# Performance work log

Hardware: AMD Instinct MI355X
Metric: run time of the kernel (lower is better)

The kernel has to match this reference:

```python
import jax, jax.numpy as jnp
import numpy as np
import math

B = 2        # batch
S = 4095     # input sequence (cls token makes L = 4096)
F_IN = 32    # input feature size
D = 512      # d_model (hidden_size)
H = 8        # n_heads
E = D // H   # head dim = 64
DFF = 2048   # feedforward dim
NL = 2       # encoder layers
FACTOR = 5   # probsparse sampling factor
EPS = 1e-5


def setup_inputs() -> dict:
    key = jax.random.key(0)
    ks = jax.random.split(key, 16)

    def w(k, shape):
        return jax.random.normal(k, shape, dtype=jnp.float32) * 0.02

    inp = {}
    inp['x'] = jax.random.normal(ks[0], (B, S, F_IN), dtype=jnp.float32)
    inp['We'] = w(ks[1], (D, F_IN)); inp['be'] = jnp.zeros((D,), jnp.float32)
    inp['cls'] = jnp.zeros((1, 1, D), jnp.float32)
    inp['Wq'] = w(ks[2], (NL, D, D)); inp['bq'] = jnp.zeros((NL, D), jnp.float32)
    inp['Wk'] = w(ks[3], (NL, D, D)); inp['bk'] = jnp.zeros((NL, D), jnp.float32)
    inp['Wv'] = w(ks[4], (NL, D, D)); inp['bv'] = jnp.zeros((NL, D), jnp.float32)
    inp['Wo'] = w(ks[5], (NL, D, D)); inp['bo'] = jnp.zeros((NL, D), jnp.float32)
    inp['g1'] = jnp.ones((NL, D), jnp.float32); inp['b1'] = jnp.zeros((NL, D), jnp.float32)
    inp['g2'] = jnp.ones((NL, D), jnp.float32); inp['b2'] = jnp.zeros((NL, D), jnp.float32)
    inp['W1'] = w(ks[6], (NL, DFF, D)); inp['bf1'] = jnp.zeros((NL, DFF), jnp.float32)
    inp['W2'] = w(ks[7], (NL, D, DFF)); inp['bf2'] = jnp.zeros((NL, D), jnp.float32)
    inp['Wf'] = w(ks[8], (1, D)); inp['bf'] = jnp.zeros((1,), jnp.float32)
    return inp


def pos_encoding(L):
    # Sinusoidal positional encoding [L, D]
    pos = jnp.arange(L, dtype=jnp.float32)[:, None]
    div = jnp.exp(jnp.arange(0, D, 2, dtype=jnp.float32) * (-math.log(10000.0) / D))
    pe = jnp.zeros((L, D), jnp.float32)
    pe = pe.at[:, 0::2].set(jnp.sin(pos * div))
    pe = pe.at[:, 1::2].set(jnp.cos(pos * div))
    return pe


def layer_norm(x, g, b):
    mu = x.mean(-1, keepdims=True)
    var = ((x - mu) ** 2).mean(-1, keepdims=True)
    return (x - mu) / jnp.sqrt(var + EPS) * g + b


def prob_attention(q, k, v, rng):
    # q, k, v: [B, H, L, E]; mask_flag=False (encoder self-attention)
    b, h, L, e = q.shape
    u = min(FACTOR * int(np.ceil(np.log(L))), L)  # sample_k == n_top here (L_Q == L_K)
    idx = jax.random.randint(rng, (L, u), 0, L)   # random K sampling per query position
    Ks = k[:, :, idx, :]                          # [B,H,L,u,E] gather
    QKs = jnp.einsum('bhle,bhlue->bhlu', q, Ks)   # sampled scores
    M = QKs.max(-1) - QKs.sum(-1) / L             # sparsity measure [B,H,L]
    _, top = jax.lax.top_k(M, u)                  # active query indices [B,H,u]
    Qr = jnp.take_along_axis(q, top[..., None], axis=2)      # [B,H,u,E]
    scores = jnp.einsum('bhue,bhke->bhuk', Qr, k) / math.sqrt(e)
    attn = jax.nn.softmax(scores, axis=-1)
    ctx = jnp.broadcast_to(v.mean(axis=2, keepdims=True), (b, h, L, e))  # initial context = mean(V)
    upd = jnp.einsum('bhuk,bhke->bhue', attn, v)
    bi = jnp.arange(b)[:, None, None]
    hi = jnp.arange(h)[None, :, None]
    ctx = ctx.at[bi, hi, top].set(upd)            # scatter active-query contexts
    return ctx                                    # [B,H,L,E]


def attention_layer(x, Wq_, bq_, Wk_, bk_, Wv_, bv_, Wo_, bo_, rng):
    b, L, _ = x.shape
    q = (x @ Wq_.T + bq_).reshape(b, L, H, E).transpose(0, 2, 1, 3)
    k = (x @ Wk_.T + bk_).reshape(b, L, H, E).transpose(0, 2, 1, 3)
    v = (x @ Wv_.T + bv_).reshape(b, L, H, E).transpose(0, 2, 1, 3)
    ctx = prob_attention(q, k, v, rng)            # [B,H,L,E]
    out = ctx.transpose(0, 2, 1, 3).reshape(b, L, D)
    return out @ Wo_.T + bo_


def reference(x, We, be, cls, Wq, bq, Wk, bk, Wv, bv, Wo, bo, g1, b1, g2, b2, W1, bf1, W2, bf2, Wf, bf):
    h = x @ We.T + be                                            # [B,S,D]
    h = jnp.concatenate([jnp.broadcast_to(cls, (B, 1, D)), h], axis=1)  # prepend cls
    L = h.shape[1]
    h = h + pos_encoding(L)[None]
    for l in range(NL):
        rng = jax.random.fold_in(jax.random.key(42), l)
        a = attention_layer(h, Wq[l], bq[l], Wk[l], bk[l], Wv[l], bv[l], Wo[l], bo[l], rng)
        h = layer_norm(h + a, g1[l], b1[l])
        y = jax.nn.relu(h @ W1[l].T + bf1[l])
        y = y @ W2[l].T + bf2[l]
        h = layer_norm(h + y, g2[l], b2[l])
    return h[:, 0] @ Wf.T + bf  # cls-token prediction head [B,1]
```

## Files before the change

### kernel.cpp

```cpp
#include <hip/hip_runtime.h>
#include <hip/hip_bf16.h>
#include <math.h>
#include <stdint.h>

#define B 2
#define S 4095
#define LSEQ 4096
#define F_IN 32
#define D 512
#define H 8
#define E 64
#define DFF 2048
#define NL 2
#define U 45
#define EPSL 1e-5f
#define LU (LSEQ * U)
#define HALF_LU (LU / 2)
#define NS 32
#define SLICE 128

typedef __attribute__((ext_vector_type(8))) short short8;
typedef __attribute__((ext_vector_type(4))) float f32x4;

#define GLD(gp, lp)                                                            \
    __builtin_amdgcn_global_load_lds(                                          \
        (const __attribute__((address_space(1))) void*)(gp),                   \
        (__attribute__((address_space(3))) void*)(lp), 16, 0, 0)

__device__ __forceinline__ unsigned short bf16_bits(float f) {
    __hip_bfloat16 h = __float2bfloat16(f);
    return *(unsigned short*)&h;
}
__device__ __forceinline__ float bits_to_f32(unsigned short s) {
    union { uint32_t u; float f; } c;
    c.u = ((uint32_t)s) << 16;
    return c.f;
}
__device__ __forceinline__ unsigned long long mkey(float v, int index) {
    uint32_t u = __float_as_uint(v);
    uint32_t mono = (u & 0x80000000u) ? ~u : (u | 0x80000000u);
    return ((unsigned long long)mono << 32) | (uint32_t)(0xFFFFFFFFu - (uint32_t)index);
}

#define TF_BODY(k0, k1, c0, c1, o0, o1)                                        \
    do {                                                                       \
        uint32_t ks2 = (k0) ^ (k1) ^ 0x1BD11BDAu;                              \
        uint32_t x0 = (c0) + (k0), x1 = (c1) + (k1);                           \
        x0 += x1; x1 = ((x1 << 13) | (x1 >> 19)); x1 ^= x0;                    \
        x0 += x1; x1 = ((x1 << 15) | (x1 >> 17)); x1 ^= x0;                    \
        x0 += x1; x1 = ((x1 << 26) | (x1 >> 6));  x1 ^= x0;                    \
        x0 += x1; x1 = ((x1 << 6) | (x1 >> 26));  x1 ^= x0;                    \
        x0 += (k1); x1 += ks2 + 1u;                                            \
        x0 += x1; x1 = ((x1 << 17) | (x1 >> 15)); x1 ^= x0;                    \
        x0 += x1; x1 = ((x1 << 29) | (x1 >> 3));  x1 ^= x0;                    \
        x0 += x1; x1 = ((x1 << 16) | (x1 >> 16)); x1 ^= x0;                    \
        x0 += x1; x1 = ((x1 << 24) | (x1 >> 8));  x1 ^= x0;                    \
        x0 += ks2; x1 += (k0) + 2u;                                            \
        x0 += x1; x1 = ((x1 << 13) | (x1 >> 19)); x1 ^= x0;                    \
        x0 += x1; x1 = ((x1 << 15) | (x1 >> 17)); x1 ^= x0;                    \
        x0 += x1; x1 = ((x1 << 26) | (x1 >> 6));  x1 ^= x0;                    \
        x0 += x1; x1 = ((x1 << 6) | (x1 >> 26));  x1 ^= x0;                    \
        x0 += (k0); x1 += (k1) + 3u;                                           \
        x0 += x1; x1 = ((x1 << 17) | (x1 >> 15)); x1 ^= x0;                    \
        x0 += x1; x1 = ((x1 << 29) | (x1 >> 3));  x1 ^= x0;                    \
        x0 += x1; x1 = ((x1 << 16) | (x1 >> 16)); x1 ^= x0;                    \
        x0 += x1; x1 = ((x1 << 24) | (x1 >> 8));  x1 ^= x0;                    \
        x0 += (k1); x1 += ks2 + 4u;                                            \
        x0 += x1; x1 = ((x1 << 13) | (x1 >> 19)); x1 ^= x0;                    \
        x0 += x1; x1 = ((x1 << 15) | (x1 >> 17)); x1 ^= x0;                    \
        x0 += x1; x1 = ((x1 << 26) | (x1 >> 6));  x1 ^= x0;                    \
        x0 += x1; x1 = ((x1 << 6) | (x1 >> 26));  x1 ^= x0;                    \
        x0 += ks2; x1 += (k0) + 5u;                                            \
        (o0) = x0; (o1) = x1;                                                  \
    } while (0)

__device__ __forceinline__ void threefry_dev(uint32_t k0, uint32_t k1, uint32_t c0,
                                             uint32_t c1, uint32_t& o0, uint32_t& o1) {
    TF_BODY(k0, k1, c0, c1, o0, o1);
}
static void threefry_host(uint32_t k0, uint32_t k1, uint32_t c0, uint32_t c1,
                          uint32_t& o0, uint32_t& o1) {
    TF_BODY(k0, k1, c0, c1, o0, o1);
}

__global__ void prep_embed_kernel(const float* __restrict__ x, const float* __restrict__ We,
                                  __hip_bfloat16* __restrict__ xbf,
                                  __hip_bfloat16* __restrict__ webf) {
    int u = blockIdx.x * blockDim.x + threadIdx.x;
    const int NX = B * LSEQ * F_IN / 4;
    const int NW = D * F_IN / 4;
    if (u < NX) {
        int e0 = u * 4;
        int i = e0 & 31;
        int l = (e0 >> 5) & (LSEQ - 1);
        int b = e0 >> 17;
        union { unsigned short s[4]; uint2 w; } o;
        if (l == 0) {
            o.s[0] = o.s[1] = o.s[2] = o.s[3] = 0;
        } else {
            float4 v = *(const float4*)(x + ((size_t)b * S + (l - 1)) * F_IN + i);
            o.s[0] = bf16_bits(v.x); o.s[1] = bf16_bits(v.y);
            o.s[2] = bf16_bits(v.z); o.s[3] = bf16_bits(v.w);
        }
        ((uint2*)xbf)[u] = o.w;
    } else if (u < NX + NW) {
        int w = u - NX;
        float4 v = ((const float4*)We)[w];
        union { unsigned short s[4]; uint2 w2; } o;
        o.s[0] = bf16_bits(v.x); o.s[1] = bf16_bits(v.y);
        o.s[2] = bf16_bits(v.z); o.s[3] = bf16_bits(v.w);
        ((uint2*)webf)[w] = o.w2;
    }
}

__global__ __launch_bounds__(256) void gemm32(const unsigned short* __restrict__ A,
                                              const unsigned short* __restrict__ W,
                                              const float* __restrict__ bias,
                                              float* __restrict__ Cf,
                                              int M, int N, int K) {
    __shared__ unsigned short lds[2 * 128 * 32];
    unsigned short* As = lds;
    unsigned short* Bs = lds + 128 * 32;
    const int tid = threadIdx.x;
    const int m0 = blockIdx.y * 128, n0 = blockIdx.x * 128;
    const int wave = tid >> 6, lane = tid & 63;
    const int wm = (wave >> 1) * 64, wn = (wave & 1) * 64;
    const int quad = lane >> 4, m15 = lane & 15;
    const int srow = tid >> 2, scol = (tid & 3) * 8;
    f32x4 acc[4][4] = {};
    const unsigned short* Ag0 = A + (size_t)(m0 + srow) * K + scol;
    const unsigned short* Ag1 = A + (size_t)(m0 + srow + 64) * K + scol;
    const unsigned short* Wg0 = W + (size_t)(n0 + srow) * K + scol;
    const unsigned short* Wg1 = W + (size_t)(n0 + srow + 64) * K + scol;
    for (int k0 = 0; k0 < K; k0 += 32) {
        __syncthreads();
        GLD(Ag0 + k0, As + tid * 8);
        GLD(Ag1 + k0, As + 2048 + tid * 8);
        GLD(Wg0 + k0, Bs + tid * 8);
        GLD(Wg1 + k0, Bs + 2048 + tid * 8);
        __syncthreads();
        short8 af[4], bfr[4];
#pragma unroll
        for (int mi = 0; mi < 4; ++mi)
            af[mi] = *(const short8*)(As + (wm + mi * 16 + m15) * 32 + quad * 8);
#pragma unroll
        for (int ni = 0; ni < 4; ++ni)
            bfr[ni] = *(const short8*)(Bs + (wn + ni * 16 + m15) * 32 + quad * 8);
#pragma unroll
        for (int mi = 0; mi < 4; ++mi)
#pragma unroll
            for (int ni = 0; ni < 4; ++ni)
                acc[mi][ni] = __builtin_amdgcn_mfma_f32_16x16x32_bf16(
                    af[mi], bfr[ni], acc[mi][ni], 0, 0, 0);
    }
#pragma unroll
    for (int mi = 0; mi < 4; ++mi) {
        int mg = m0 + wm + mi * 16 + quad * 4;
#pragma unroll
        for (int ni = 0; ni < 4; ++ni) {
            int ng = n0 + wn + ni * 16 + m15;
            float bv = bias[ng];
#pragma unroll
            for (int r = 0; r < 4; ++r)
                Cf[(size_t)(mg + r) * N + ng] = acc[mi][ni][r] + bv;
        }
    }
}

__global__ void posenc_kernel(const float* __restrict__ emb, const float* __restrict__ cls,
                              __hip_bfloat16* __restrict__ hbf) {
    int gid = blockIdx.x * blockDim.x + threadIdx.x;
    if (gid >= B * LSEQ * D) return;
    int d = gid % D;
    int l = (gid / D) % LSEQ;
    float v = (l == 0) ? cls[d] : emb[gid];
    int i = d >> 1;
    float divv = expf((float)(2 * i) * (float)(-9.210340371976184 / 512.0));
    float ang = (float)l * divv;
    v += (d & 1) ? cosf(ang) : sinf(ang);
    hbf[gid] = __float2bfloat16(v);
}

__global__ void cast_weights_kernel(const float* __restrict__ Wq_l,
                                    const float* __restrict__ Wk_l,
                                    const float* __restrict__ Wv_l,
                                    const float* __restrict__ Wo_l,
                                    const float* __restrict__ W1_l,
                                    const float* __restrict__ W2_l,
                                    const float* __restrict__ bq_l,
                                    const float* __restrict__ bk_l,
                                    const float* __restrict__ bv_l,
                                    __hip_bfloat16* __restrict__ wqb,
                                    __hip_bfloat16* __restrict__ wkb,
                                    __hip_bfloat16* __restrict__ wvb,
                                    __hip_bfloat16* __restrict__ wob,
                                    __hip_bfloat16* __restrict__ w1b,
                                    __hip_bfloat16* __restrict__ w2b,
                                    float* __restrict__ qkvbias,
                                    unsigned char* __restrict__ flags) {
    const int SDD = D * D / 4;
    const int SFD = DFF * D / 4;
    const int CAST_N = 4 * SDD + 2 * SFD;
    int u = blockIdx.x * blockDim.x + threadIdx.x;
    if (u >= CAST_N) {
        int j = u - CAST_N;
        if (j < 384) {
            int seg = (j * 4) >> 9;
            int off = (j * 4) & 511;
            const float* src = (seg == 0) ? bq_l : (seg == 1) ? bk_l : bv_l;
            *(float4*)(qkvbias + j * 4) = *(const float4*)(src + off);
        } else if (j < 384 + B * LSEQ / 4) {
            ((int*)flags)[j - 384] = 0;
        }
        return;
    }
    const float* src;
    __hip_bfloat16* dst;
    int off;
    if (u < SDD) { src = Wq_l; dst = wqb; off = u; }
    else if (u < 2 * SDD) { src = Wk_l; dst = wkb; off = u - SDD; }
    else if (u < 3 * SDD) { src = Wv_l; dst = wvb; off = u - 2 * SDD; }
    else if (u < 4 * SDD) { src = Wo_l; dst = wob; off = u - 3 * SDD; }
    else if (u < 4 * SDD + SFD) { src = W1_l; dst = w1b; off = u - 4 * SDD; }
    else { src = W2_l; dst = w2b; off = u - 4 * SDD - SFD; }
    float4 v = ((const float4*)src)[off];
    union { unsigned short s[4]; uint2 w; } o;
    o.s[0] = bf16_bits(v.x); o.s[1] = bf16_bits(v.y);
    o.s[2] = bf16_bits(v.z); o.s[3] = bf16_bits(v.w);
    ((uint2*)dst)[off] = o.w;
}

template <int MODE>
__global__ __launch_bounds__(256) void gemm_pipe(const unsigned short* __restrict__ A,
                                                 const unsigned short* __restrict__ W,
                                                 const float* __restrict__ bias,
                                                 void* __restrict__ C0,
                                                 void* __restrict__ C1,
                                                 void* __restrict__ C2,
                                                 int M, int N, int K, int NBN) {
    __shared__ unsigned short As[2][128 * 32];
    __shared__ unsigned short Bs[2][128 * 32];
    const int tid = threadIdx.x;
    const int NBM = M >> 7;
    const int bid = blockIdx.x;
    const int xcd = bid & 7, local = bid >> 3;
    const int m_t = xcd * (NBM >> 3) + local / NBN;
    const int n_t = local % NBN;
    const int m0 = m_t * 128, n0 = n_t * 128;
    const int wave = tid >> 6, lane = tid & 63;
    const int wm = (wave >> 1) * 64, wn = (wave & 1) * 64;
    const int quad = lane >> 4, m15 = lane & 15;
    const int srow = tid >> 2, scol = (tid & 3) * 8;
    f32x4 acc[4][4] = {};
    const unsigned short* Ag0 = A + (size_t)(m0 + srow) * K + scol;
    const unsigned short* Ag1 = A + (size_t)(m0 + srow + 64) * K + scol;
    const unsigned short* Wg0 = W + (size_t)(n0 + srow) * K + scol;
    const unsigned short* Wg1 = W + (size_t)(n0 + srow + 64) * K + scol;
    GLD(Ag0, As[0] + tid * 8);
    GLD(Ag1, As[0] + 2048 + tid * 8);
    GLD(Wg0, Bs[0] + tid * 8);
    GLD(Wg1, Bs[0] + 2048 + tid * 8);
    int cur = 0;
    for (int k0 = 0; k0 < K; k0 += 32) {
        __syncthreads();
        int kn = k0 + 32;
        if (kn < K) {
            GLD(Ag0 + kn, As[cur ^ 1] + tid * 8);
            GLD(Ag1 + kn, As[cur ^ 1] + 2048 + tid * 8);
            GLD(Wg0 + kn, Bs[cur ^ 1] + tid * 8);
            GLD(Wg1 + kn, Bs[cur ^ 1] + 2048 + tid * 8);
        }
        short8 af[4], bfr[4];
#pragma unroll
        for (int mi = 0; mi < 4; ++mi)
            af[mi] = *(const short8*)(As[cur] + (wm + mi * 16 + m15) * 32 + quad * 8);
#pragma unroll
        for (int ni = 0; ni < 4; ++ni)
            bfr[ni] = *(const short8*)(Bs[cur] + (wn + ni * 16 + m15) * 32 + quad * 8);
#pragma unroll
        for (int mi = 0; mi < 4; ++mi)
#pragma unroll
            for (int ni = 0; ni < 4; ++ni)
                acc[mi][ni] = __builtin_amdgcn_mfma_f32_16x16x32_bf16(
                    af[mi], bfr[ni], acc[mi][ni], 0, 0, 0);
        cur ^= 1;
    }
#pragma unroll
    for (int mi = 0; mi < 4; ++mi) {
        int mg = m0 + wm + mi * 16 + quad * 4;
#pragma unroll
        for (int ni = 0; ni < 4; ++ni) {
            int ng = n0 + wn + ni * 16 + m15;
            float bv = bias[ng];
#pragma unroll
            for (int r = 0; r < 4; ++r) {
                float v = acc[mi][ni][r] + bv;
                if (MODE == 1) {
                    ((__hip_bfloat16*)C0)[(size_t)(mg + r) * N + ng] = __float2bfloat16(v);
                } else if (MODE == 2) {
                    ((__hip_bfloat16*)C0)[(size_t)(mg + r) * N + ng] =
                        __float2bfloat16(fmaxf(v, 0.f));
                } else {
                    int seg = ng >> 9;
                    int col = ng & 511;
                    __hip_bfloat16* dst = (seg == 0) ? (__hip_bfloat16*)C0
                                        : (seg == 1) ? (__hip_bfloat16*)C1
                                                     : (__hip_bfloat16*)C2;
                    dst[(size_t)(mg + r) * D + col] = __float2bfloat16(v);
                }
            }
        }
    }
}

__global__ __launch_bounds__(256) void gemm_w2b(const unsigned short* __restrict__ A,
                                                const unsigned short* __restrict__ W,
                                                const float* __restrict__ bias,
                                                float* __restrict__ C0,
                                                float* __restrict__ C1) {
    const int K = 2048, N = 512, KH = 1024;
    __shared__ unsigned short As[2][128 * 32];
    __shared__ unsigned short Bs[2][128 * 32];
    const int tid = threadIdx.x;
    const int bid = blockIdx.x;
    const int xcd = bid & 7, local = bid >> 3;
    const int m_t = xcd * 8 + (local >> 3);
    const int n_t = (local >> 1) & 3;
    const int ks = local & 1;
    const int m0 = m_t * 128, n0 = n_t * 128, kb = ks * KH;
    const int wave = tid >> 6, lane = tid & 63;
    const int wm = (wave >> 1) * 64, wn = (wave & 1) * 64;
    const int quad = lane >> 4, m15 = lane & 15;
    const int srow = tid >> 2, scol = (tid & 3) * 8;
    f32x4 acc[4][4] = {};
    const unsigned short* Ag0 = A + (size_t)(m0 + srow) * K + kb + scol;
    const unsigned short* Ag1 = A + (size_t)(m0 + srow + 64) * K + kb + scol;
    const unsigned short* Wg0 = W + (size_t)(n0 + srow) * K + kb + scol;
    const unsigned short* Wg1 = W + (size_t)(n0 + srow + 64) * K + kb + scol;
    GLD(Ag0, As[0] + tid * 8);
    GLD(Ag1, As[0] + 2048 + tid * 8);
    GLD(Wg0, Bs[0] + tid * 8);
    GLD(Wg1, Bs[0] + 2048 + tid * 8);
    int cur = 0;
    for (int k0 = 0; k0 < KH; k0 += 32) {
        __syncthreads();
        int kn = k0 + 32;
        if (kn < KH) {
            GLD(Ag0 + kn, As[cur ^ 1] + tid * 8);
            GLD(Ag1 + kn, As[cur ^ 1] + 2048 + tid * 8);
            GLD(Wg0 + kn, Bs[cur ^ 1] + tid * 8);
            GLD(Wg1 + kn, Bs[cur ^ 1] + 2048 + tid * 8);
        }
        short8 af[4], bfr[4];
#pragma unroll
        for (int mi = 0; mi < 4; ++mi)
            af[mi] = *(const short8*)(As[cur] + (wm + mi * 16 + m15) * 32 + quad * 8);
#pragma unroll
        for (int ni = 0; ni < 4; ++ni)
            bfr[ni] = *(const short8*)(Bs[cur] + (wn + ni * 16 + m15) * 32 + quad * 8);
#pragma unroll
        for (int mi = 0; mi < 4; ++mi)
#pragma unroll
            for (int ni = 0; ni < 4; ++ni)
                acc[mi][ni] = __builtin_amdgcn_mfma_f32_16x16x32_bf16(
                    af[mi], bfr[ni], acc[mi][ni], 0, 0, 0);
        cur ^= 1;
    }
    float* Cf = ks ? C1 : C0;
#pragma unroll
    for (int mi = 0; mi < 4; ++mi) {
        int mg = m0 + wm + mi * 16 + quad * 4;
#pragma unroll
        for (int ni = 0; ni < 4; ++ni) {
            int ng = n0 + wn + ni * 16 + m15;
            float bv = ks ? 0.f : bias[ng];
#pragma unroll
            for (int r = 0; r < 4; ++r)
                Cf[(size_t)(mg + r) * N + ng] = acc[mi][ni][r] + bv;
        }
    }
}

__global__ __launch_bounds__(256) void mscore_kernel(const __hip_bfloat16* __restrict__ qbf,
                                                     const __hip_bfloat16* __restrict__ kbf,
                                                     uint32_t k2a, uint32_t k2b,
                                                     float* __restrict__ Mv) {
    __shared__ float Sbuf[U][8];
    __shared__ int sidx[U];
    int bid = blockIdx.x;
    int b = bid & 1;
    int l = bid >> 1;
    int tid = threadIdx.x;
    int wave = tid >> 6, lane = tid & 63;
    if (tid < U) {
        int i = l * U + tid;
        uint32_t c0 = (i < HALF_LU) ? (uint32_t)i : (uint32_t)(i - HALF_LU);
        uint32_t o0, o1;
        threefry_dev(k2a, k2b, c0, c0 + HALF_LU, o0, o1);
        sidx[tid] = (int)(((i < HALF_LU) ? o0 : o1) & 4095u);
    }
    const unsigned short* qr =
        (const unsigned short*)qbf + ((size_t)(b * LSEQ) + l) * D + lane * 8;
    union { uint4 u; unsigned short s[8]; } qv;
    qv.u = *(const uint4*)qr;
    float qa[8];
#pragma unroll
    for (int j = 0; j < 8; ++j) qa[j] = bits_to_f32(qv.s[j]);
    __syncthreads();
    const unsigned short* kbase = (const unsigned short*)(kbf + (size_t)(b * LSEQ) * D);
    for (int t = wave; t < U; t += 4) {
        int kr = sidx[t];
        union { uint4 u; unsigned short s[8]; } kv;
        kv.u = *(const uint4*)(kbase + (size_t)kr * D + lane * 8);
        float p = 0.f;
#pragma unroll
        for (int j = 0; j < 8; ++j) p += qa[j] * bits_to_f32(kv.s[j]);
        p += __shfl_xor(p, 1);
        p += __shfl_xor(p, 2);
        p += __shfl_xor(p, 4);
        if ((lane & 7) == 0) Sbuf[t][lane >> 3] = p;
    }
    __syncthreads();
    if (tid < 8) {
        float mx = -INFINITY, sm = 0.f;
        for (int t = 0; t < U; ++t) {
            float v = Sbuf[t][tid];
            mx = fmaxf(mx, v);
            sm += v;
        }
        Mv[((size_t)b * H + tid) * LSEQ + l] = mx - sm / (float)LSEQ;
    }
}

__global__ __launch_bounds__(256) void topk_chunk_kernel(const float* __restrict__ Mv,
                                                         unsigned long long* __restrict__ cand) {
    __shared__ unsigned long long sk[256];
    int blk = blockIdx.x;
    int chunk = blk & 15, bh = blk >> 4;
    int tid = threadIdx.x;
    int gi = chunk * 256 + tid;
    sk[tid] = mkey(Mv[(size_t)bh * LSEQ + gi], gi);
    __syncthreads();
    for (int k = 2; k <= 256; k <<= 1) {
        for (int j = k >> 1; j > 0; j >>= 1) {
            int ixj = tid ^ j;
            if (ixj > tid) {
                unsigned long long a = sk[tid], b = sk[ixj];
                bool desc = ((tid & k) == 0);
                if (desc ? (a < b) : (a > b)) { sk[tid] = b; sk[ixj] = a; }
            }
            __syncthreads();
        }
    }
    if (tid < U) cand[((size_t)bh * 16 + chunk) * U + tid] = sk[tid];
}

__global__ __launch_bounds__(256) void topkmerge_vmean_kernel(
        const unsigned long long* __restrict__ cand, int* __restrict__ top,
        const __hip_bfloat16* __restrict__ v, float* __restrict__ part) {
    __shared__ unsigned long long sk[1024];
    __shared__ float red[4][64];
    int blk = blockIdx.x;
    int tid = threadIdx.x;
    if (blk < B * H) {
        int bh = blk;
        for (int e = tid; e < 1024; e += 256)
            sk[e] = (e < 16 * U) ? cand[(size_t)bh * 16 * U + e] : 0ull;
        __syncthreads();
        for (int k = 2; k <= 1024; k <<= 1) {
            for (int j = k >> 1; j > 0; j >>= 1) {
                for (int e = tid; e < 1024; e += 256) {
                    int ixj = e ^ j;
                    if (ixj > e) {
                        unsigned long long a = sk[e], b = sk[ixj];
                        bool desc = ((e & k) == 0);
                        if (desc ? (a < b) : (a > b)) { sk[e] = b; sk[ixj] = a; }
                    }
                }
                __syncthreads();
            }
        }
        if (tid < U)
            top[bh * U + tid] = (int)(0xFFFFFFFFu - (uint32_t)(sk[tid] & 0xFFFFFFFFu));
    } else {
        int vb = blk - B * H;
        int seg = vb & 7, hh = (vb >> 3) & 7, b = vb >> 6;
        int e = tid & 63, rg = tid >> 6;
        const __hip_bfloat16* vp =
            v + ((size_t)(b * LSEQ) + seg * 512) * D + hh * 64 + e;
        float acc = 0.f;
        for (int r = rg; r < 512; r += 4) acc += __bfloat162float(vp[(size_t)r * D]);
        red[rg][e] = acc;
        __syncthreads();
        if (tid < 64)
            part[(size_t)vb * 64 + tid] =
                red[0][tid] + red[1][tid] + red[2][tid] + red[3][tid];
    }
}

__global__ __launch_bounds__(256) void zero_wobase_kernel(
        const int* __restrict__ top, float* __restrict__ aout,
        unsigned char* __restrict__ flags, const float* __restrict__ vpart,
        const unsigned short* __restrict__ wob, const float* __restrict__ bo,
        float* __restrict__ base) {
    int bid = blockIdx.x;
    int tid = threadIdx.x;
    if (bid < B * H * U) {
        int t = bid % U;
        int bh = bid / U;
        int b = bh >> 3;
        int r = top[bh * U + t];
        if (tid < 128) {
            float4 z = {0.f, 0.f, 0.f, 0.f};
            ((float4*)(aout + (size_t)(b * LSEQ + r) * D))[tid] = z;
        }
        if (tid == 0) flags[b * LSEQ + r] = 1;
    } else {
        int wb = bid - B * H * U;
        int b = wb >> 7;
        int n = (wb & 127) * 4 + (tid >> 6);
        int lane = tid & 63;
        float vmv[8];
#pragma unroll
        for (int j = 0; j < 8; ++j) {
            int idx = lane * 8 + j;
            int hh = idx >> 6, e = idx & 63;
            float acc = 0.f;
#pragma unroll
            for (int s = 0; s < 8; ++s)
                acc += vpart[((size_t)(b * 8 + hh) * 8 + s) * 64 + e];
            vmv[j] = acc / (float)LSEQ;
        }
        union { uint4 u; unsigned short s[8]; } w;
        w.u = *(const uint4*)(wob + (size_t)n * D + lane * 8);
        float p = vmv[0] * bits_to_f32(w.s[0]) + vmv[1] * bits_to_f32(w.s[1]) +
                  vmv[2] * bits_to_f32(w.s[2]) + vmv[3] * bits_to_f32(w.s[3]) +
                  vmv[4] * bits_to_f32(w.s[4]) + vmv[5] * bits_to_f32(w.s[5]) +
                  vmv[6] * bits_to_f32(w.s[6]) + vmv[7] * bits_to_f32(w.s[7]);
        for (int off = 32; off; off >>= 1) p += __shfl_xor(p, off);
        if (lane == 0) base[(size_t)b * D + n] = p + bo[n];
    }
}

__global__ __launch_bounds__(256) void attnred_corr_kernel(const float* __restrict__ Opart,
                                                           const float* __restrict__ msum,
                                                           const float* __restrict__ vpart,
                                                           const unsigned short* __restrict__ wob,
                                                           const int* __restrict__ top,
                                                           float* __restrict__ aout) {
    __shared__ float dlt[E];
    int bid = blockIdx.x;
    int t = bid % U;
    int bh = bid / U;
    int b = bh >> 3, hh = bh & 7;
    int tid = threadIdx.x;
    if (tid < 64) {
        int lane = tid;
        float m_s = -INFINITY, ss = 0.f;
        if (lane < NS) {
            size_t base = (((size_t)bh * NS + lane) * U + t) * 2;
            m_s = msum[base];
            ss = msum[base + 1];
        }
        float M = m_s;
        for (int off = 32; off; off >>= 1) M = fmaxf(M, __shfl_xor(M, off));
        float e_s = (lane < NS) ? __expf(m_s - M) : 0.f;
        float d = ss * e_s;
        for (int off = 32; off; off >>= 1) d += __shfl_xor(d, off);
        float acc = 0.f;
        for (int s = 0; s < NS; ++s) {
            float w = __shfl(e_s, s);
            acc += w * Opart[(((size_t)bh * NS + s) * U + t) * 64 + lane];
        }
        float vmv = 0.f;
#pragma unroll
        for (int s = 0; s < 8; ++s) vmv += vpart[((size_t)bh * 8 + s) * 64 + lane];
        dlt[lane] = acc / d - vmv / (float)LSEQ;
    }
    __syncthreads();
    int r = top[bh * U + t];
    float* arow = aout + (size_t)(b * LSEQ + r) * D;
    for (int n = tid; n < D; n += 256) {
        const unsigned short* wr = wob + (size_t)n * D + hh * E;
        float acc = 0.f;
#pragma unroll
        for (int k2 = 0; k2 < E; ++k2) acc += dlt[k2] * bits_to_f32(wr[k2]);
        atomicAdd(arow + n, acc);
    }
}

__global__ __launch_bounds__(256) void attn_part(const __hip_bfloat16* __restrict__ qbf,
                                                 const __hip_bfloat16* __restrict__ kbf,
                                                 const __hip_bfloat16* __restrict__ vbf,
                                                 const int* __restrict__ top,
                                                 float* __restrict__ Opart,
                                                 float* __restrict__ msum) {
    __shared__ unsigned short Qs[48 * 72];
    __shared__ unsigned short Ks[SLICE * 72];
    __shared__ unsigned short Vs[SLICE * 68];
    __shared__ unsigned short Ps[48 * 136];
    __shared__ float mred[48][4];
    __shared__ float sred[48][4];
    const int slice = blockIdx.x, hh = blockIdx.y, b = blockIdx.z;
    const int bh = b * H + hh;
    const int tid = threadIdx.x;
    const int s0 = slice * SLICE;
    for (int i = tid; i < 48 * 64; i += 256) {
        int t = i >> 6, e = i & 63;
        unsigned short v = 0;
        if (t < U) {
            int r = top[bh * U + t];
            v = ((const unsigned short*)qbf)[((size_t)(b * LSEQ) + r) * D + hh * E + e];
        }
        Qs[t * 72 + e] = v;
    }
    {
        const uint4* src = (const uint4*)(kbf + ((size_t)(b * LSEQ) + s0) * D + hh * E);
        for (int i = tid; i < SLICE * 8; i += 256) {
            int r = i >> 3, c = i & 7;
            uint4 d = src[(size_t)r * 64 + c];
            *(uint4*)(Ks + r * 72 + c * 8) = d;
        }
    }
    {
        const uint2* src = (const uint2*)(vbf + ((size_t)(b * LSEQ) + s0) * D + hh * E);
        for (int i = tid; i < SLICE * 16; i += 256) {
            int r = i >> 4, c = i & 15;
            uint2 d = src[(size_t)r * 128 + c];
            *(uint2*)(Vs + r * 68 + c * 4) = d;
        }
    }
    __syncthreads();
    const int wave = tid >> 6, lane = tid & 63;
    const int quad = lane >> 4, m15 = lane & 15;
    const int wc = wave * 32;
    f32x4 acc[3][2] = {};
#pragma unroll
    for (int ks = 0; ks < 2; ++ks) {
        short8 af[3], bfr[2];
#pragma unroll
        for (int mt = 0; mt < 3; ++mt)
            af[mt] = *(const short8*)(Qs + (mt * 16 + m15) * 72 + ks * 32 + quad * 8);
#pragma unroll
        for (int nt = 0; nt < 2; ++nt)
            bfr[nt] = *(const short8*)(Ks + (wc + nt * 16 + m15) * 72 + ks * 32 + quad * 8);
#pragma unroll
        for (int mt = 0; mt < 3; ++mt)
#pragma unroll
            for (int nt = 0; nt < 2; ++nt)
                acc[mt][nt] = __builtin_amdgcn_mfma_f32_16x16x32_bf16(
                    af[mt], bfr[nt], acc[mt][nt], 0, 0, 0);
    }
    float sc[3][2][4];
#pragma unroll
    for (int mt = 0; mt < 3; ++mt)
#pragma unroll
        for (int nt = 0; nt < 2; ++nt)
#pragma unroll
            for (int r = 0; r < 4; ++r) sc[mt][nt][r] = acc[mt][nt][r] * 0.125f;
#pragma unroll
    for (int mt = 0; mt < 3; ++mt)
#pragma unroll
        for (int r = 0; r < 4; ++r) {
            float mv = fmaxf(sc[mt][0][r], sc[mt][1][r]);
            mv = fmaxf(mv, __shfl_xor(mv, 1));
            mv = fmaxf(mv, __shfl_xor(mv, 2));
            mv = fmaxf(mv, __shfl_xor(mv, 4));
            mv = fmaxf(mv, __shfl_xor(mv, 8));
            if (m15 == 0) mred[mt * 16 + quad * 4 + r][wave] = mv;
        }
    __syncthreads();
#pragma unroll
    for (int mt = 0; mt < 3; ++mt)
#pragma unroll
        for (int r = 0; r < 4; ++r) {
            int row = mt * 16 + quad * 4 + r;
            float ms = fmaxf(fmaxf(mred[row][0], mred[row][1]),
                             fmaxf(mred[row][2], mred[row][3]));
            float p0 = __expf(sc[mt][0][r] - ms);
            float p1 = __expf(sc[mt][1][r] - ms);
            float sv = p0 + p1;
            sv += __shfl_xor(sv, 1);
            sv += __shfl_xor(sv, 2);
            sv += __shfl_xor(sv, 4);
            sv += __shfl_xor(sv, 8);
            if (m15 == 0) sred[row][wave] = sv;
            Ps[row * 136 + wc + m15] = bf16_bits(p0);
            Ps[row * 136 + wc + 16 + m15] = bf16_bits(p1);
        }
    __syncthreads();
    if (tid < U) {
        float mm = fmaxf(fmaxf(mred[tid][0], mred[tid][1]),
                         fmaxf(mred[tid][2], mred[tid][3]));
        float ss = sred[tid][0] + sred[tid][1] + sred[tid][2] + sred[tid][3];
        size_t base = (((size_t)bh * NS + slice) * U + tid) * 2;
        msum[base] = mm;
        msum[base + 1] = ss;
    }
    f32x4 apv[3] = {};
#pragma unroll
    for (int ks = 0; ks < 4; ++ks) {
        short8 bv;
#pragma unroll
        for (int j = 0; j < 8; ++j)
            bv[j] = (short)Vs[(ks * 32 + quad * 8 + j) * 68 + wave * 16 + m15];
        short8 af2[3];
#pragma unroll
        for (int mt = 0; mt < 3; ++mt)
            af2[mt] = *(const short8*)(Ps + (mt * 16 + m15) * 136 + ks * 32 + quad * 8);
#pragma unroll
        for (int mt = 0; mt < 3; ++mt)
            apv[mt] = __builtin_amdgcn_mfma_f32_16x16x32_bf16(af2[mt], bv, apv[mt], 0, 0, 0);
    }
    size_t obase = ((size_t)bh * NS + slice) * U;
#pragma unroll
    for (int mt = 0; mt < 3; ++mt)
#pragma unroll
        for (int r = 0; r < 4; ++r) {
            int row = mt * 16 + quad * 4 + r;
            if (row < U)
                Opart[(obase + row) * 64 + wave * 16 + m15] = apv[mt][r];
        }
}

__global__ __launch_bounds__(64) void add_ln_base_kernel(__hip_bfloat16* __restrict__ hbf,
                                                         const float* __restrict__ base,
                                                         const float* __restrict__ aout,
                                                         const unsigned char* __restrict__ flags,
                                                         const float* __restrict__ g,
                                                         const float* __restrict__ bb) {
    int row = blockIdx.x;
    int b = row >> 12;
    int lane = threadIdx.x;
    unsigned short* hp = (unsigned short*)hbf + (size_t)row * D;
    const float* bp = base + (size_t)b * D;
    const float* ap = aout + (size_t)row * D;
    bool has = flags[row] != 0;
    float x[8];
    float sum = 0.f;
#pragma unroll
    for (int j = 0; j < 8; ++j) {
        float a = bp[lane + 64 * j];
        if (has) a += ap[lane + 64 * j];
        x[j] = bits_to_f32(hp[lane + 64 * j]) + a;
        sum += x[j];
    }
    for (int off = 32; off; off >>= 1) sum += __shfl_xor(sum, off);
    float mu = sum / (float)D;
    float vs = 0.f;
#pragma unroll
    for (int j = 0; j < 8; ++j) {
        float dd = x[j] - mu;
        vs += dd * dd;
    }
    for (int off = 32; off; off >>= 1) vs += __shfl_xor(vs, off);
    float inv = 1.f / sqrtf(vs / (float)D + EPSL);
#pragma unroll
    for (int j = 0; j < 8; ++j) {
        float o = (x[j] - mu) * inv * g[lane + 64 * j] + bb[lane + 64 * j];
        hp[lane + 64 * j] = bf16_bits(o);
    }
}

__global__ __launch_bounds__(64) void add_ln_kernel(__hip_bfloat16* __restrict__ hbf,
                                                    const float* __restrict__ a,
                                                    const float* __restrict__ a2,
                                                    const float* __restrict__ g,
                                                    const float* __restrict__ bb) {
    int row = blockIdx.x;
    int lane = threadIdx.x;
    unsigned short* hp = (unsigned short*)hbf + (size_t)row * D;
    const float* ap = a + (size_t)row * D;
    const float* ap2 = a2 + (size_t)row * D;
    float x[8];
    float sum = 0.f;
#pragma unroll
    for (int j = 0; j < 8; ++j) {
        x[j] = bits_to_f32(hp[lane + 64 * j]) + ap[lane + 64 * j] + ap2[lane + 64 * j];
        sum += x[j];
    }
    for (int off = 32; off; off >>= 1) sum += __shfl_xor(sum, off);
    float mu = sum / (float)D;
    float vs = 0.f;
#pragma unroll
    for (int j = 0; j < 8; ++j) {
        float dd = x[j] - mu;
        vs += dd * dd;
    }
    for (int off = 32; off; off >>= 1) vs += __shfl_xor(vs, off);
    float inv = 1.f / sqrtf(vs / (float)D + EPSL);
#pragma unroll
    for (int j = 0; j < 8; ++j) {
        float o = (x[j] - mu) * inv * g[lane + 64 * j] + bb[lane + 64 * j];
        hp[lane + 64 * j] = bf16_bits(o);
    }
}

__global__ void final_kernel(const __hip_bfloat16* __restrict__ hbf,
                             const float* __restrict__ Wf,
                             const float* __restrict__ bf, float* __restrict__ out) {
    int b = blockIdx.x;
    int lane = threadIdx.x;
    const unsigned short* hp = (const unsigned short*)hbf + (size_t)b * LSEQ * D;
    float acc = 0.f;
    for (int j = lane; j < D; j += 64) acc += bits_to_f32(hp[j]) * Wf[j];
    for (int off = 32; off; off >>= 1) acc += __shfl_xor(acc, off);
    if (lane == 0) out[b] = acc + bf[0];
}

extern "C" void kernel_launch(void* const* d_in, const int* in_sizes, int n_in,
                              void* d_out, int out_size, void* d_ws, size_t ws_size,
                              hipStream_t stream) {
    (void)in_sizes; (void)n_in; (void)out_size; (void)ws_size;
    const float* x   = (const float*)d_in[0];
    const float* We  = (const float*)d_in[1];
    const float* be  = (const float*)d_in[2];
    const float* cls = (const float*)d_in[3];
    const float* Wq  = (const float*)d_in[4];
    const float* bq  = (const float*)d_in[5];
    const float* Wk  = (const float*)d_in[6];
    const float* bk  = (const float*)d_in[7];
    const float* Wv  = (const float*)d_in[8];
    const float* bv  = (const float*)d_in[9];
    const float* Wo  = (const float*)d_in[10];
    const float* bo  = (const float*)d_in[11];
    const float* g1  = (const float*)d_in[12];
    const float* b1  = (const float*)d_in[13];
    const float* g2  = (const float*)d_in[14];
    const float* b2  = (const float*)d_in[15];
    const float* W1  = (const float*)d_in[16];
    const float* bf1 = (const float*)d_in[17];
    const float* W2  = (const float*)d_in[18];
    const float* bf2 = (const float*)d_in[19];
    const float* Wf  = (const float*)d_in[20];
    const float* bff = (const float*)d_in[21];
    float* out = (float*)d_out;

    float* ws = (float*)d_ws;
    const size_t NT = (size_t)B * LSEQ * D;
    float* aout = ws + NT;
    __hip_bfloat16* kbf    = (__hip_bfloat16*)(ws + NT);
    __hip_bfloat16* q_bf   = (__hip_bfloat16*)(ws + 2 * NT);
    __hip_bfloat16* y1_bf  = (__hip_bfloat16*)(ws + 2 * NT);
    __hip_bfloat16* v_bf   = (__hip_bfloat16*)(ws + 4 * NT);
    __hip_bfloat16* h_bf   = (__hip_bfloat16*)(ws + 5 * NT);
    float* emb  = ws;
    float* tmp  = ws;
    float* Opart = ws + 3 * NT;
    float* msumb = Opart + (size_t)B * H * NS * U * 64;
    float* wpool = ws + 5 * NT + NT / 2;
    __hip_bfloat16* wqb = (__hip_bfloat16*)wpool;
    __hip_bfloat16* wkb = wqb + (size_t)D * D;
    __hip_bfloat16* wvb = wkb + (size_t)D * D;
    __hip_bfloat16* wob = wvb + (size_t)D * D;
    __hip_bfloat16* w1b = wob + (size_t)D * D;
    __hip_bfloat16* w2b = w1b + (size_t)DFF * D;
    float* after_w = wpool + ((size_t)4 * D * D + 2 * (size_t)DFF * D) / 2;
    float* Mbuf = after_w;
    int* top    = (int*)(Mbuf + (size_t)B * H * LSEQ);
    float* vm   = (float*)(top + B * H * U);
    float* vpart  = vm + (size_t)B * H * E;
    float* baseb  = vpart + (size_t)128 * 64;
    __hip_bfloat16* xbf  = (__hip_bfloat16*)(baseb + (size_t)B * D);
    __hip_bfloat16* webf = xbf + (size_t)B * LSEQ * F_IN;
    unsigned long long* cand =
        (unsigned long long*)(((uintptr_t)(webf + (size_t)D * F_IN) + 7) & ~(uintptr_t)7);
    float* qkvbias = (float*)(cand + (size_t)B * H * 16 * U);
    unsigned char* flags = (unsigned char*)(qkvbias + 1536);

    const int ML = B * LSEQ;
    dim3 gD(D / 128, ML / 128);
    const int CAST_N = 4 * (D * D / 4) + 2 * (DFF * D / 4);
    const int CAST_TOT = CAST_N + 384 + B * LSEQ / 4;

    prep_embed_kernel<<<(B * LSEQ * F_IN / 4 + D * F_IN / 4 + 255) / 256, 256, 0, stream>>>(
        x, We, xbf, webf);
    gemm32<<<gD, 256, 0, stream>>>((const unsigned short*)xbf,
                                   (const unsigned short*)webf, be, emb, ML, D, F_IN);
    posenc_kernel<<<(B * LSEQ * D + 255) / 256, 256, 0, stream>>>(emb, cls, h_bf);

    for (int l = 0; l < NL; ++l) {
        uint32_t f0, f1, a0, a1, bb0, bb1;
        threefry_host(0u, 42u, 0u, (uint32_t)l, f0, f1);
        threefry_host(f0, f1, 0u, 2u, a0, a1);
        threefry_host(f0, f1, 1u, 3u, bb0, bb1);
        (void)a0; (void)bb0;

        cast_weights_kernel<<<(CAST_TOT + 255) / 256, 256, 0, stream>>>(
            Wq + (size_t)l * D * D, Wk + (size_t)l * D * D, Wv + (size_t)l * D * D,
            Wo + (size_t)l * D * D, W1 + (size_t)l * DFF * D, W2 + (size_t)l * D * DFF,
            bq + l * D, bk + l * D, bv + l * D,
            wqb, wkb, wvb, wob, w1b, w2b, qkvbias, flags);

        gemm_pipe<3><<<768, 256, 0, stream>>>((const unsigned short*)h_bf,
                                              (const unsigned short*)wqb, qkvbias,
                                              q_bf, kbf, v_bf, ML, 3 * D, D, 12);

        mscore_kernel<<<B * LSEQ, 256, 0, stream>>>(q_bf, kbf, a1, bb1, Mbuf);
        topk_chunk_kernel<<<B * H * 16, 256, 0, stream>>>(Mbuf, cand);
        topkmerge_vmean_kernel<<<B * H + B * H * 8, 256, 0, stream>>>(cand, top, v_bf,
                                                                      vpart);
        attn_part<<<dim3(NS, H, B), 256, 0, stream>>>(q_bf, kbf, v_bf, top, Opart, msumb);
        zero_wobase_kernel<<<B * H * U + B * 128, 256, 0, stream>>>(
            top, aout, flags, vpart, (const unsigned short*)wob, bo + l * D, baseb);
        attnred_corr_kernel<<<B * H * U, 256, 0, stream>>>(Opart, msumb, vpart,
                                                           (const unsigned short*)wob, top,
                                                           aout);
        add_ln_base_kernel<<<ML, 64, 0, stream>>>(h_bf, baseb, aout, flags,
                                                  g1 + l * D, b1 + l * D);

        gemm_pipe<2><<<1024, 256, 0, stream>>>((const unsigned short*)h_bf,
                                               (const unsigned short*)w1b, bf1 + l * DFF,
                                               y1_bf, nullptr, nullptr, ML, DFF, D, 16);
        gemm_w2b<<<512, 256, 0, stream>>>((const unsigned short*)y1_bf,
                                          (const unsigned short*)w2b, bf2 + l * D,
                                          aout, tmp);
        add_ln_kernel<<<ML, 64, 0, stream>>>(h_bf, aout, tmp, g2 + l * D, b2 + l * D);
    }

    final_kernel<<<B, 64, 0, stream>>>(h_bf, Wf, bff, out);
}
```

Baseline: 553.0 us.

## Hoist weight casting for both layers into one launch and batch K-row loads

Weight and bias casting for both layers now runs in a single 2D-grid launch before the layer loop, with per-layer bf16 slices in a larger pool. This removes one kernel launch per layer. The flag zeroing moves into extra blocks of the top-k merge kernel. The mscore kernel issues three sampled-K row loads per iteration before reducing them, to hide memory latency, and the Wo correction loop reads 16-byte vectors instead of scalars. The weight pool grows to hold both layers.

```diff
diff --git a/kernel.cpp b/kernel.cpp
--- a/kernel.cpp
+++ b/kernel.cpp
@@ -181,48 +181,44 @@
     hbf[gid] = __float2bfloat16(v);
 }
 
-__global__ void cast_weights_kernel(const float* __restrict__ Wq_l,
-                                    const float* __restrict__ Wk_l,
-                                    const float* __restrict__ Wv_l,
-                                    const float* __restrict__ Wo_l,
-                                    const float* __restrict__ W1_l,
-                                    const float* __restrict__ W2_l,
-                                    const float* __restrict__ bq_l,
-                                    const float* __restrict__ bk_l,
-                                    const float* __restrict__ bv_l,
-                                    __hip_bfloat16* __restrict__ wqb,
-                                    __hip_bfloat16* __restrict__ wkb,
-                                    __hip_bfloat16* __restrict__ wvb,
-                                    __hip_bfloat16* __restrict__ wob,
-                                    __hip_bfloat16* __restrict__ w1b,
-                                    __hip_bfloat16* __restrict__ w2b,
-                                    float* __restrict__ qkvbias,
-                                    unsigned char* __restrict__ flags) {
+__global__ void cast_weights_kernel(const float* __restrict__ Wq,
+                                    const float* __restrict__ Wk,
+                                    const float* __restrict__ Wv,
+                                    const float* __restrict__ Wo,
+                                    const float* __restrict__ W1,
+                                    const float* __restrict__ W2,
+                                    const float* __restrict__ bq,
+                                    const float* __restrict__ bk,
+                                    const float* __restrict__ bv,
+                                    __hip_bfloat16* __restrict__ wpool,
+                                    float* __restrict__ qkvbias) {
     const int SDD = D * D / 4;
     const int SFD = DFF * D / 4;
     const int CAST_N = 4 * SDD + 2 * SFD;
+    const size_t WPL = (size_t)4 * D * D + 2 * (size_t)DFF * D;
+    int l = blockIdx.y;
     int u = blockIdx.x * blockDim.x + threadIdx.x;
+    __hip_bfloat16* base = wpool + (size_t)l * WPL;
     if (u >= CAST_N) {
         int j = u - CAST_N;
         if (j < 384) {
             int seg = (j * 4) >> 9;
             int off = (j * 4) & 511;
-            const float* src = (seg == 0) ? bq_l : (seg == 1) ? bk_l : bv_l;
-            *(float4*)(qkvbias + j * 4) = *(const float4*)(src + off);
-        } else if (j < 384 + B * LSEQ / 4) {
-            ((int*)flags)[j - 384] = 0;
+            const float* src = (seg == 0) ? bq + l * D
+                             : (seg == 1) ? bk + l * D : bv + l * D;
+            *(float4*)(qkvbias + l * 1536 + j * 4) = *(const float4*)(src + off);
         }
         return;
     }
     const float* src;
     __hip_bfloat16* dst;
     int off;
-    if (u < SDD) { src = Wq_l; dst = wqb; off = u; }
-    else if (u < 2 * SDD) { src = Wk_l; dst = wkb; off = u - SDD; }
-    else if (u < 3 * SDD) { src = Wv_l; dst = wvb; off = u - 2 * SDD; }
-    else if (u < 4 * SDD) { src = Wo_l; dst = wob; off = u - 3 * SDD; }
-    else if (u < 4 * SDD + SFD) { src = W1_l; dst = w1b; off = u - 4 * SDD; }
-    else { src = W2_l; dst = w2b; off = u - 4 * SDD - SFD; }
+    if (u < SDD)            { src = Wq + (size_t)l * D * D;   dst = base;                       off = u; }
+    else if (u < 2 * SDD)   { src = Wk + (size_t)l * D * D;   dst = base + (size_t)D * D;       off = u - SDD; }
+    else if (u < 3 * SDD)   { src = Wv + (size_t)l * D * D;   dst = base + (size_t)2 * D * D;   off = u - 2 * SDD; }
+    else if (u < 4 * SDD)   { src = Wo + (size_t)l * D * D;   dst = base + (size_t)3 * D * D;   off = u - 3 * SDD; }
+    else if (u < 4 * SDD + SFD) { src = W1 + (size_t)l * DFF * D; dst = base + (size_t)4 * D * D; off = u - 4 * SDD; }
+    else { src = W2 + (size_t)l * D * DFF; dst = base + (size_t)4 * D * D + (size_t)DFF * D; off = u - 4 * SDD - SFD; }
     float4 v = ((const float4*)src)[off];
     union { unsigned short s[4]; uint2 w; } o;
     o.s[0] = bf16_bits(v.x); o.s[1] = bf16_bits(v.y);
@@ -408,17 +404,40 @@
     for (int j = 0; j < 8; ++j) qa[j] = bits_to_f32(qv.s[j]);
     __syncthreads();
     const unsigned short* kbase = (const unsigned short*)(kbf + (size_t)(b * LSEQ) * D);
-    for (int t = wave; t < U; t += 4) {
-        int kr = sidx[t];
-        union { uint4 u; unsigned short s[8]; } kv;
-        kv.u = *(const uint4*)(kbase + (size_t)kr * D + lane * 8);
-        float p = 0.f;
-#pragma unroll
-        for (int j = 0; j < 8; ++j) p += qa[j] * bits_to_f32(kv.s[j]);
-        p += __shfl_xor(p, 1);
-        p += __shfl_xor(p, 2);
-        p += __shfl_xor(p, 4);
-        if ((lane & 7) == 0) Sbuf[t][lane >> 3] = p;
+    for (int t = wave; t < U; t += 12) {
+        int tb = t + 4, tc = t + 8;
+        bool hb = tb < U, hc = tc < U;
+        union { uint4 u; unsigned short s[8]; } kva, kvb, kvc;
+        kva.u = *(const uint4*)(kbase + (size_t)sidx[t] * D + lane * 8);
+        if (hb) kvb.u = *(const uint4*)(kbase + (size_t)sidx[tb] * D + lane * 8);
+        if (hc) kvc.u = *(const uint4*)(kbase + (size_t)sidx[tc] * D + lane * 8);
+        {
+            float p = 0.f;
+#pragma unroll
+            for (int j = 0; j < 8; ++j) p += qa[j] * bits_to_f32(kva.s[j]);
+            p += __shfl_xor(p, 1);
+            p += __shfl_xor(p, 2);
+            p += __shfl_xor(p, 4);
+            if ((lane & 7) == 0) Sbuf[t][lane >> 3] = p;
+        }
+        if (hb) {
+            float p = 0.f;
+#pragma unroll
+            for (int j = 0; j < 8; ++j) p += qa[j] * bits_to_f32(kvb.s[j]);
+            p += __shfl_xor(p, 1);
+            p += __shfl_xor(p, 2);
+            p += __shfl_xor(p, 4);
+            if ((lane & 7) == 0) Sbuf[tb][lane >> 3] = p;
+        }
+        if (hc) {
+            float p = 0.f;
+#pragma unroll
+            for (int j = 0; j < 8; ++j) p += qa[j] * bits_to_f32(kvc.s[j]);
+            p += __shfl_xor(p, 1);
+            p += __shfl_xor(p, 2);
+            p += __shfl_xor(p, 4);
+            if ((lane & 7) == 0) Sbuf[tc][lane >> 3] = p;
+        }
     }
     __syncthreads();
     if (tid < 8) {
@@ -457,7 +476,8 @@
 
 __global__ __launch_bounds__(256) void topkmerge_vmean_kernel(
         const unsigned long long* __restrict__ cand, int* __restrict__ top,
-        const __hip_bfloat16* __restrict__ v, float* __restrict__ part) {
+        const __hip_bfloat16* __restrict__ v, float* __restrict__ part,
+        unsigned char* __restrict__ flags) {
     __shared__ unsigned long long sk[1024];
     __shared__ float red[4][64];
     int blk = blockIdx.x;
@@ -482,7 +502,7 @@
         }
         if (tid < U)
             top[bh * U + tid] = (int)(0xFFFFFFFFu - (uint32_t)(sk[tid] & 0xFFFFFFFFu));
-    } else {
+    } else if (blk < B * H + B * H * 8) {
         int vb = blk - B * H;
         int seg = vb & 7, hh = (vb >> 3) & 7, b = vb >> 6;
         int e = tid & 63, rg = tid >> 6;
@@ -495,6 +515,9 @@
         if (tid < 64)
             part[(size_t)vb * 64 + tid] =
                 red[0][tid] + red[1][tid] + red[2][tid] + red[3][tid];
+    } else {
+        int fb = blk - (B * H + B * H * 8);
+        ((int*)flags)[fb * 256 + tid] = 0;
     }
 }
 
@@ -584,7 +607,13 @@
         const unsigned short* wr = wob + (size_t)n * D + hh * E;
         float acc = 0.f;
 #pragma unroll
-        for (int k2 = 0; k2 < E; ++k2) acc += dlt[k2] * bits_to_f32(wr[k2]);
+        for (int v4 = 0; v4 < 8; ++v4) {
+            union { uint4 u; unsigned short s[8]; } w;
+            w.u = *(const uint4*)(wr + v4 * 8);
+#pragma unroll
+            for (int j = 0; j < 8; ++j)
+                acc += dlt[v4 * 8 + j] * bits_to_f32(w.s[j]);
+        }
         atomicAdd(arow + n, acc);
     }
 }
@@ -849,13 +878,9 @@
     float* Opart = ws + 3 * NT;
     float* msumb = Opart + (size_t)B * H * NS * U * 64;
     float* wpool = ws + 5 * NT + NT / 2;
-    __hip_bfloat16* wqb = (__hip_bfloat16*)wpool;
-    __hip_bfloat16* wkb = wqb + (size_t)D * D;
-    __hip_bfloat16* wvb = wkb + (size_t)D * D;
-    __hip_bfloat16* wob = wvb + (size_t)D * D;
-    __hip_bfloat16* w1b = wob + (size_t)D * D;
-    __hip_bfloat16* w2b = w1b + (size_t)DFF * D;
-    float* after_w = wpool + ((size_t)4 * D * D + 2 * (size_t)DFF * D) / 2;
+    const size_t WPL = (size_t)4 * D * D + 2 * (size_t)DFF * D;
+    __hip_bfloat16* wpool_bf = (__hip_bfloat16*)wpool;
+    float* after_w = wpool + (2 * WPL) / 2;
     float* Mbuf = after_w;
     int* top    = (int*)(Mbuf + (size_t)B * H * LSEQ);
     float* vm   = (float*)(top + B * H * U);
@@ -866,15 +891,17 @@
     unsigned long long* cand =
         (unsigned long long*)(((uintptr_t)(webf + (size_t)D * F_IN) + 7) & ~(uintptr_t)7);
     float* qkvbias = (float*)(cand + (size_t)B * H * 16 * U);
-    unsigned char* flags = (unsigned char*)(qkvbias + 1536);
+    unsigned char* flags = (unsigned char*)(qkvbias + 2 * 1536);
 
     const int ML = B * LSEQ;
     dim3 gD(D / 128, ML / 128);
     const int CAST_N = 4 * (D * D / 4) + 2 * (DFF * D / 4);
-    const int CAST_TOT = CAST_N + 384 + B * LSEQ / 4;
+    dim3 gCast((CAST_N + 384 + 255) / 256, NL);
 
     prep_embed_kernel<<<(B * LSEQ * F_IN / 4 + D * F_IN / 4 + 255) / 256, 256, 0, stream>>>(
         x, We, xbf, webf);
+    cast_weights_kernel<<<gCast, 256, 0, stream>>>(Wq, Wk, Wv, Wo, W1, W2, bq, bk, bv,
+                                                   wpool_bf, qkvbias);
     gemm32<<<gD, 256, 0, stream>>>((const unsigned short*)xbf,
                                    (const unsigned short*)webf, be, emb, ML, D, F_IN);
     posenc_kernel<<<(B * LSEQ * D + 255) / 256, 256, 0, stream>>>(emb, cls, h_bf);
@@ -886,20 +913,20 @@
         threefry_host(f0, f1, 1u, 3u, bb0, bb1);
         (void)a0; (void)bb0;
 
-        cast_weights_kernel<<<(CAST_TOT + 255) / 256, 256, 0, stream>>>(
-            Wq + (size_t)l * D * D, Wk + (size_t)l * D * D, Wv + (size_t)l * D * D,
-            Wo + (size_t)l * D * D, W1 + (size_t)l * DFF * D, W2 + (size_t)l * D * DFF,
-            bq + l * D, bk + l * D, bv + l * D,
-            wqb, wkb, wvb, wob, w1b, w2b, qkvbias, flags);
+        __hip_bfloat16* wqb = wpool_bf + (size_t)l * WPL;
+        __hip_bfloat16* wob = wqb + (size_t)3 * D * D;
+        __hip_bfloat16* w1b = wqb + (size_t)4 * D * D;
+        __hip_bfloat16* w2b = w1b + (size_t)DFF * D;
 
         gemm_pipe<3><<<768, 256, 0, stream>>>((const unsigned short*)h_bf,
-                                              (const unsigned short*)wqb, qkvbias,
+                                              (const unsigned short*)wqb,
+                                              qkvbias + (size_t)l * 1536,
                                               q_bf, kbf, v_bf, ML, 3 * D, D, 12);
 
         mscore_kernel<<<B * LSEQ, 256, 0, stream>>>(q_bf, kbf, a1, bb1, Mbuf);
         topk_chunk_kernel<<<B * H * 16, 256, 0, stream>>>(Mbuf, cand);
-        topkmerge_vmean_kernel<<<B * H + B * H * 8, 256, 0, stream>>>(cand, top, v_bf,
-                                                                      vpart);
+        topkmerge_vmean_kernel<<<B * H + B * H * 8 + 8, 256, 0, stream>>>(
+            cand, top, v_bf, vpart, flags);
         attn_part<<<dim3(NS, H, B), 256, 0, stream>>>(q_bf, kbf, v_bf, top, Opart, msumb);
         zero_wobase_kernel<<<B * H * U + B * 128, 256, 0, stream>>>(
             top, aout, flags, vpart, (const unsigned short*)wob, bo + l * D, baseb);
```

Measured after the change: 544.5 us. No clear change (-1.5%).
